# Kernel optimization log

Measured on AMD Instinct MI355X. Metric: run time of the kernel, lower is better.

## Reference

```python
import jax, jax.numpy as jnp
import numpy as np

WS = (7, 7, 7)
SS = (3, 3, 3)
SEQ = WS[0] * WS[1] * WS[2]  # 343
EPS = 1e-5


def layer_norm(x, w, b):
    mu = jnp.mean(x, axis=-1, keepdims=True)
    var = jnp.mean((x - mu) ** 2, axis=-1, keepdims=True)
    return (x - mu) * jax.lax.rsqrt(var + EPS) * w + b


def window_partition(x, ws):
    b, d, h, w, c = x.shape
    x = x.reshape(b, d // ws[0], ws[0], h // ws[1], ws[1], w // ws[2], ws[2], c)
    return x.transpose(0, 1, 3, 5, 2, 4, 6, 7).reshape(-1, ws[0] * ws[1] * ws[2], c)


def window_reverse(win, ws, dims):
    b, dp, hp, wp = dims
    x = win.reshape(b, dp // ws[0], hp // ws[1], wp // ws[2], ws[0], ws[1], ws[2], -1)
    return x.transpose(0, 1, 4, 2, 5, 3, 6, 7).reshape(b, dp, hp, wp, -1)


def _rel_pos_index():
    coords = np.stack(np.meshgrid(np.arange(WS[0]), np.arange(WS[1]), np.arange(WS[2]), indexing='ij'))
    cf = coords.reshape(3, -1)
    rel = (cf[:, :, None] - cf[:, None, :]).transpose(1, 2, 0)  # (s, s, 3)
    rel[..., 0] += WS[0] - 1
    rel[..., 1] += WS[1] - 1
    rel[..., 2] += WS[2] - 1
    idx = rel[..., 0] * (2 * WS[1] - 1) * (2 * WS[2] - 1) + rel[..., 1] * (2 * WS[2] - 1) + rel[..., 2]
    return idx.astype(np.int32)


def _swin_mask(dp, hp, wp):
    img = np.zeros((1, dp, hp, wp, 1), np.float32)
    cnt = 0
    sl = lambda ws, ss: (slice(0, -ws), slice(-ws, -ss), slice(-ss, None))
    for ds in sl(WS[0], SS[0]):
        for hs in sl(WS[1], SS[1]):
            for wsl in sl(WS[2], SS[2]):
                img[:, ds, hs, wsl, :] = cnt
                cnt += 1
    mw = np.asarray(window_partition(jnp.asarray(img), WS)).squeeze(-1)  # (nW, s)
    am = mw[:, None, :] - mw[:, :, None]
    return np.where(am != 0, np.float32(-100.0), np.float32(0.0))


def setup_inputs() -> dict:
    key = jax.random.key(0)
    ks = jax.random.split(key, 12)
    B, D, H, W, C = 1, 28, 56, 28, 192
    NH, DH = 6, 32
    FFI = 4 * C
    L = 2
    s = 0.02
    inp = {
        'x': jax.random.normal(ks[0], (B, D, H, W, C), jnp.float32),
        'mask_matrix': jnp.asarray(_swin_mask(D, H, W)),
        'clinical': jax.random.normal(ks[1], (B, 8), jnp.float32),
        'ln1_w': jnp.ones((L, C)), 'ln1_b': jnp.zeros((L, C)),
        'qkv_w': jax.random.normal(ks[2], (L, C, 3 * C)) * s, 'qkv_b': jnp.zeros((L, 3 * C)),
        'out_w': jax.random.normal(ks[3], (L, C, C)) * s, 'out_b': jnp.zeros((L, C)),
        'ln2_w': jnp.ones((L, C)), 'ln2_b': jnp.zeros((L, C)),
        'ff1_w': jax.random.normal(ks[4], (L, C, 2 * FFI)) * s, 'ff1_b': jnp.zeros((L, 2 * FFI)),
        'ff2_w': jax.random.normal(ks[5], (L, FFI, C)) * s, 'ff2_b': jnp.zeros((L, C)),
        'rpb': jax.random.normal(ks[6], (L, (2 * WS[0] - 1) * (2 * WS[1] - 1) * (2 * WS[2] - 1), NH)) * s,
        'lnf_w': jnp.ones((C,)), 'lnf_b': jnp.zeros((C,)),
        'rel_index': jnp.asarray(_rel_pos_index()),
    }
    return inp


def reference(x, mask_matrix, clinical, ln1_w, ln1_b, qkv_w, qkv_b, out_w, out_b,
              ln2_w, ln2_b, ff1_w, ff1_b, ff2_w, ff2_b, rpb, lnf_w, lnf_b, rel_index):
    b, d, h, w, c = x.shape
    nh = rpb.shape[-1]
    dh = c // nh
    # pad to window multiples (no-op for chosen shapes, kept for fidelity)
    pd = (WS[0] - d % WS[0]) % WS[0]
    ph = (WS[1] - h % WS[1]) % WS[1]
    pw = (WS[2] - w % WS[2]) % WS[2]
    xp = jnp.pad(x, ((0, 0), (0, pd), (0, ph), (0, pw), (0, 0)))
    dp, hp, wp = d + pd, h + ph, w + pw
    # cyclic shift
    xs = jnp.roll(xp, shift=(-SS[0], -SS[1], -SS[2]), axis=(1, 2, 3))
    xw = window_partition(xs, WS)  # (nW*b, s, c)
    # mask: values {0,-100} -> allowed bool (True = attend), per source math
    allowed = jnp.logical_not((mask_matrix * (-1.0 / 100.0)).astype(bool))[:, None, :, :]
    scale = 1.0 / jnp.sqrt(jnp.asarray(dh, xw.dtype))
    for l in range(2):
        hdn = layer_norm(xw, ln1_w[l], ln1_b[l])
        qkv = hdn @ qkv_w[l] + qkv_b[l]
        q, k, v = jnp.split(qkv, 3, axis=-1)
        q = q.reshape(-1, SEQ, nh, dh).transpose(0, 2, 1, 3)
        k = k.reshape(-1, SEQ, nh, dh).transpose(0, 2, 1, 3)
        v = v.reshape(-1, SEQ, nh, dh).transpose(0, 2, 1, 3)
        scores = jnp.einsum('whqd,whkd->whqk', q, k) * scale
        bias = rpb[l][rel_index].transpose(2, 0, 1)  # (nh, s, s)
        scores = scores + bias[None]
        scores = jnp.where(allowed, scores, jnp.asarray(-1e9, scores.dtype))
        attn = jax.nn.softmax(scores, axis=-1)
        o = jnp.einsum('whqk,whkd->whqd', attn, v).transpose(0, 2, 1, 3).reshape(-1, SEQ, c)
        xw = xw + (o @ out_w[l] + out_b[l])
        f = layer_norm(xw, ln2_w[l], ln2_b[l]) @ ff1_w[l] + ff1_b[l]
        u, g = jnp.split(f, 2, axis=-1)  # GLU feed-forward
        xw = xw + ((u * jax.nn.gelu(g)) @ ff2_w[l] + ff2_b[l])
    xw = layer_norm(xw, lnf_w, lnf_b)
    aw = xw.reshape(-1, WS[0], WS[1], WS[2], c)
    xs = window_reverse(aw, WS, (b, dp, hp, wp))
    xo = jnp.roll(xs, shift=(SS[0], SS[1], SS[2]), axis=(1, 2, 3))
    return xo[:, :d, :h, :w, :]
```

## Files before the change

### kernel.cpp

```cpp
#include <hip/hip_runtime.h>
#include <hip/hip_fp16.h>
#include <math.h>

#define SEQ 343
#define CCH 192
#define NWIN 128
#define NHEAD 6
#define TOK (NWIN * SEQ)

typedef __bf16 bf16x8 __attribute__((ext_vector_type(8)));
typedef float f32x4 __attribute__((ext_vector_type(4)));
typedef float f32x16 __attribute__((ext_vector_type(16)));
typedef unsigned short ushort8 __attribute__((ext_vector_type(8)));
typedef _Float16 half8 __attribute__((ext_vector_type(8)));
typedef _Float16 half4 __attribute__((ext_vector_type(4)));

__device__ __forceinline__ unsigned short f2bf(float f) {
    unsigned u = __float_as_uint(f);
    u += 0x7FFF + ((u >> 16) & 1);
    return (unsigned short)(u >> 16);
}

__device__ __forceinline__ float gelu_tanh(float x) {
    const float k0 = 0.7978845608028654f;
    const float k1 = 0.044715f;
    float y = k0 * (x + k1 * x * x * x);
    float t = 1.0f - 2.0f / (__expf(2.0f * y) + 1.0f);
    return 0.5f * x * (1.0f + t);
}

__device__ __forceinline__ void gld16(void* l, const void* g) {
    __builtin_amdgcn_global_load_lds((const __attribute__((address_space(1))) unsigned int*)g,
                                     (__attribute__((address_space(3))) unsigned int*)l, 16, 0, 0);
}

__global__ __launch_bounds__(256) void k_shift_part(const float* __restrict__ x,
                                                    float* __restrict__ xw) {
    int idx = blockIdx.x * 256 + threadIdx.x;
    if (idx >= TOK * 48) return;
    int c4 = idx % 48;
    int tok = idx / 48;
    int t = tok % SEQ;
    int wn = tok / SEQ;
    int tw = t % 7, th = (t / 7) % 7, td = t / 49;
    int ww = wn & 3, wh = (wn >> 2) & 7, wd = wn >> 5;
    int sd = (wd * 7 + td + 3) % 28;
    int sh = (wh * 7 + th + 3) % 56;
    int sw = (ww * 7 + tw + 3) % 28;
    const float4* src = (const float4*)(x + (size_t)((sd * 56 + sh) * 28 + sw) * CCH);
    ((float4*)xw)[idx] = src[c4];
}

__global__ __launch_bounds__(256) void k_ln_bf(const float* __restrict__ in,
                                               const float* __restrict__ w,
                                               const float* __restrict__ b,
                                               unsigned short* __restrict__ out, int rows) {
    int row = blockIdx.x * 4 + (threadIdx.x >> 6);
    int lane = threadIdx.x & 63;
    if (row >= rows) return;
    const float* p = in + (size_t)row * CCH;
    float v0 = p[lane], v1 = p[lane + 64], v2 = p[lane + 128];
    float s = v0 + v1 + v2;
#pragma unroll
    for (int off = 32; off > 0; off >>= 1) s += __shfl_xor(s, off);
    float mu = s * (1.0f / 192.0f);
    float d0 = v0 - mu, d1 = v1 - mu, d2 = v2 - mu;
    float vv = d0 * d0 + d1 * d1 + d2 * d2;
#pragma unroll
    for (int off = 32; off > 0; off >>= 1) vv += __shfl_xor(vv, off);
    float rs = rsqrtf(vv * (1.0f / 192.0f) + 1e-5f);
    unsigned short* q = out + (size_t)row * CCH;
    q[lane] = f2bf(d0 * rs * w[lane] + b[lane]);
    q[lane + 64] = f2bf(d1 * rs * w[lane + 64] + b[lane + 64]);
    q[lane + 128] = f2bf(d2 * rs * w[lane + 128] + b[lane + 128]);
}

__global__ __launch_bounds__(256) void k_ln_out(const float* __restrict__ xw,
                                                const float* __restrict__ w,
                                                const float* __restrict__ b,
                                                float* __restrict__ out) {
    int row = blockIdx.x * 4 + (threadIdx.x >> 6);
    int lane = threadIdx.x & 63;
    if (row >= TOK) return;
    int d = row / 1568;
    int hh = (row / 28) % 56;
    int wv = row % 28;
    int sd = (d + 25) % 28, sh = (hh + 53) % 56, sw = (wv + 25) % 28;
    int wn = (sd / 7) * 32 + (sh / 7) * 4 + (sw / 7);
    int t = (sd % 7) * 49 + (sh % 7) * 7 + (sw % 7);
    const float* p = xw + ((size_t)wn * SEQ + t) * CCH;
    float v0 = p[lane], v1 = p[lane + 64], v2 = p[lane + 128];
    float s = v0 + v1 + v2;
#pragma unroll
    for (int off = 32; off > 0; off >>= 1) s += __shfl_xor(s, off);
    float mu = s * (1.0f / 192.0f);
    float d0 = v0 - mu, d1 = v1 - mu, d2 = v2 - mu;
    float vv = d0 * d0 + d1 * d1 + d2 * d2;
#pragma unroll
    for (int off = 32; off > 0; off >>= 1) vv += __shfl_xor(vv, off);
    float rs = rsqrtf(vv * (1.0f / 192.0f) + 1e-5f);
    float* q = out + (size_t)row * CCH;
    q[lane] = d0 * rs * w[lane] + b[lane];
    q[lane + 64] = d1 * rs * w[lane + 64] + b[lane + 64];
    q[lane + 128] = d2 * rs * w[lane + 128] + b[lane + 128];
}

__global__ __launch_bounds__(256) void k_wprep(const float* __restrict__ qkv_w,
                                               const float* __restrict__ out_w,
                                               const float* __restrict__ ff1_w,
                                               const float* __restrict__ ff2_w,
                                               unsigned short* __restrict__ wt) {
    int idx = blockIdx.x * 256 + threadIdx.x;
    if (idx >= 1179648) return;
    int l = idx / 589824;
    int r = idx - l * 589824;
    const float* src;
    int Kd, Nd, off;
    if (r < 110592)      { src = qkv_w + (size_t)l * 110592; Kd = 192; Nd = 576;  off = r; }
    else if (r < 147456) { src = out_w + (size_t)l * 36864;  Kd = 192; Nd = 192;  off = r - 110592; }
    else if (r < 442368) { src = ff1_w + (size_t)l * 294912; Kd = 192; Nd = 1536; off = r - 147456; }
    else                 { src = ff2_w + (size_t)l * 147456; Kd = 768; Nd = 192;  off = r - 442368; }
    int n = off / Kd, k = off - n * Kd;
    wt[idx] = f2bf(src[(size_t)k * Nd + n]);
}

__global__ void k_cbgen2(const float* __restrict__ mask, const float* __restrict__ rpb,
                         unsigned* __restrict__ cb) {
    int q = threadIdx.x;
    int kp = blockIdx.x;
    int h = blockIdx.y;
    int cl = blockIdx.z;
    int wn = ((cl & 4) ? 96 : 0) + ((cl & 2) ? 28 : 0) + ((cl & 1) ? 3 : 0);
    const float LOG2E = 1.4426950408889634f;
    int qd = q / 49, qh = (q / 7) % 7, qw = q % 7;
    unsigned short v[2];
#pragma unroll
    for (int t = 0; t < 2; ++t) {
        int k = 2 * kp + t;
        float val = -14000.0f;
        if (k < SEQ && q < SEQ) {
            float mk = mask[((size_t)wn * SEQ + k) * SEQ + q];
            if (mk == 0.0f) {
                int kd = k / 49, kh = (k / 7) % 7, kw = k % 7;
                int rel = (qd - kd + 6) * 169 + (qh - kh + 6) * 13 + (qw - kw + 6);
                val = rpb[(size_t)rel * NHEAD + h] * LOG2E;
            }
        }
        v[t] = __half_as_ushort(__float2half_rn(val));
    }
    cb[((size_t)(cl * NHEAD + h) * 176 + kp) * 352 + q] = (unsigned)v[0] | ((unsigned)v[1] << 16);
}

template <int MODE>
__global__ __launch_bounds__(256) void k_gemm32(const unsigned short* __restrict__ A,
                                                const unsigned short* __restrict__ Wt,
                                                const float* __restrict__ bias,
                                                float* __restrict__ outF,
                                                unsigned short* __restrict__ outB,
                                                _Float16* __restrict__ outH,
                                                _Float16* __restrict__ outV,
                                                int N, int K) {
    constexpr int BN = (MODE == 0) ? 192 : 64;
    constexpr int NF = (MODE == 0) ? 3 : 1;
    constexpr int WNC = NF * 32;
    constexpr int BROWS = (MODE == 0) ? 192 : ((MODE == 2) ? 128 : 64);
    constexpr int BCH = (BROWS * 128) / 4096;
    __shared__ char AsB[16384];
    __shared__ char BsB[BROWS * 128];
    const int tid = threadIdx.x;
    const int n0 = blockIdx.x * BN;
    const size_t m0 = (size_t)blockIdx.y * 128;
    const int lane = tid & 63, wid = tid >> 6;
    const int wm = wid >> 1, wn = wid & 1;
    const int ln31 = lane & 31, hi16 = (lane >> 5) * 16;
    const int xorv = (ln31 & 7) << 4;
    const size_t ldb = (size_t)K * 2;

    f32x16 acc[2][NF];
    f32x16 accG[2];
#pragma unroll
    for (int mi = 0; mi < 2; ++mi) {
#pragma unroll
        for (int nj = 0; nj < NF; ++nj) acc[mi][nj] = (f32x16)(0.f);
        accG[mi] = (f32x16)(0.f);
    }

    for (int kb = 0; kb < K; kb += 64) {
#pragma unroll
        for (int i = 0; i < 4; ++i) {
            int s = i * 4096 + tid * 16;
            int r = s >> 7;
            int cb = (s & 127) ^ ((r & 7) << 4);
            gld16(AsB + s, (const char*)A + (m0 + r) * ldb + (size_t)kb * 2 + cb);
        }
#pragma unroll
        for (int i = 0; i < BCH; ++i) {
            int s = i * 4096 + tid * 16;
            int r = s >> 7;
            int cb = (s & 127) ^ ((r & 7) << 4);
            int grow = n0 + r + ((MODE == 2 && r >= 64) ? 704 : 0);
            gld16(BsB + s, (const char*)Wt + (size_t)grow * ldb + (size_t)kb * 2 + cb);
        }
        __syncthreads();
#pragma unroll
        for (int ks = 0; ks < 4; ++ks) {
            const int ccb = (ks * 32 + hi16) ^ xorv;
            bf16x8 a0 = *(const bf16x8*)(AsB + (wm * 64 + ln31) * 128 + ccb);
            bf16x8 a1 = *(const bf16x8*)(AsB + (wm * 64 + 32 + ln31) * 128 + ccb);
            if (MODE == 2) {
                bf16x8 bu = *(const bf16x8*)(BsB + (wn * 32 + ln31) * 128 + ccb);
                bf16x8 bg = *(const bf16x8*)(BsB + (64 + wn * 32 + ln31) * 128 + ccb);
                acc[0][0] = __builtin_amdgcn_mfma_f32_32x32x16_bf16(a0, bu, acc[0][0], 0, 0, 0);
                acc[1][0] = __builtin_amdgcn_mfma_f32_32x32x16_bf16(a1, bu, acc[1][0], 0, 0, 0);
                accG[0] = __builtin_amdgcn_mfma_f32_32x32x16_bf16(a0, bg, accG[0], 0, 0, 0);
                accG[1] = __builtin_amdgcn_mfma_f32_32x32x16_bf16(a1, bg, accG[1], 0, 0, 0);
            } else {
#pragma unroll
                for (int nj = 0; nj < NF; ++nj) {
                    bf16x8 b = *(const bf16x8*)(BsB + (wn * WNC + nj * 32 + ln31) * 128 + ccb);
                    acc[0][nj] = __builtin_amdgcn_mfma_f32_32x32x16_bf16(a0, b, acc[0][nj], 0, 0, 0);
                    acc[1][nj] = __builtin_amdgcn_mfma_f32_32x32x16_bf16(a1, b, acc[1][nj], 0, 0, 0);
                }
            }
        }
        __syncthreads();
    }

    const float S2LOG = 0.17677669529663687f * 1.4426950408889634f;
    const int rbase = (int)m0 + wm * 64 + ((lane >> 5) << 2);
    const int cbase = n0 + wn * WNC + ln31;
#pragma unroll
    for (int mi = 0; mi < 2; ++mi) {
#pragma unroll
        for (int nj = 0; nj < NF; ++nj) {
            const int gc = cbase + nj * 32;
            const float bb = bias[gc];
            const float bgv = (MODE == 2) ? bias[768 + gc] : 0.f;
#pragma unroll
            for (int reg = 0; reg < 16; ++reg) {
                const int row = rbase + mi * 32 + (reg & 3) + ((reg >> 2) << 3);
                float v = acc[mi][nj][reg] + bb;
                if (MODE == 1) {
                    outF[(size_t)row * N + gc] += v;
                } else if (MODE == 0) {
                    if (n0 < 384) {
                        outH[(size_t)row * 384 + gc] = (_Float16)(n0 == 0 ? v * S2LOG : v);
                    } else {
                        int d = gc - 384, hh = d >> 5, dd = d & 31;
                        int wnn = row / 343, qq = row - wnn * 343;
                        outV[(((size_t)wnn * NHEAD + hh) * 32 + dd) * 344 + qq] = (_Float16)v;
                    }
                } else {
                    float g = accG[mi][reg] + bgv;
                    outB[(size_t)row * 768 + gc] = f2bf(v * gelu_tanh(g));
                }
            }
        }
    }
}

__global__ __launch_bounds__(256) void k_attn3(const _Float16* __restrict__ qk,
                                               const _Float16* __restrict__ vt,
                                               const unsigned* __restrict__ cb,
                                               unsigned short* __restrict__ o) {
    __shared__ _Float16 Ks[352][40];
    __shared__ _Float16 Vt[32][360];
    __shared__ _Float16 Pb[4][48][16][4];
    const int h = blockIdx.x;
    const int wn = blockIdx.y;
    const int tid = threadIdx.x;
    const _Float16* kbase = qk + (size_t)wn * SEQ * 384 + 192 + h * 32;
    for (int j = tid; j < 352 * 4; j += 256) {
        int s = j >> 2, c = (j & 3) * 8;
        half8 v = {};
        if (s < SEQ) v = *(const half8*)&kbase[(size_t)s * 384 + c];
        *(half8*)&Ks[s][c] = v;
    }
    const _Float16* vbase = vt + ((size_t)wn * NHEAD + h) * 32 * 344;
    for (int j = tid; j < 32 * 44; j += 256) {
        int d = j / 44, c = (j % 44) * 8;
        half8 v = {};
        if (c + 7 <= 342) {
            v = *(const half8*)&vbase[(size_t)d * 344 + c];
        } else if (c <= 342) {
#pragma unroll
            for (int i = 0; i < 8; ++i) v[i] = (c + i <= 342) ? vbase[(size_t)d * 344 + c + i] : (_Float16)0.f;
        }
        *(half8*)&Vt[d][c] = v;
    }
    __syncthreads();
    const int wid = tid >> 6, lane = tid & 63;
    const int qloc = lane & 15, g = lane >> 4;
    int cls = (((wn >> 5) == 3) ? 4 : 0) | ((((wn >> 2) & 7) == 7) ? 2 : 0) | (((wn & 3) == 3) ? 1 : 0);
    const unsigned* cbb = cb + (size_t)(cls * NHEAD + h) * 176 * 352;
    for (int qt = wid; qt < 22; qt += 4) {
        const int q0 = qt * 16;
        const int qrow = q0 + qloc;
        half8 qf = {};
        if (qrow < SEQ) qf = *(const half8*)&qk[((size_t)wn * SEQ + qrow) * 384 + h * 32 + g * 8];
        f32x4 st[22];
#pragma unroll
        for (int kt = 0; kt < 22; ++kt) {
            half8 kf = *(const half8*)&Ks[kt * 16 + qloc][g * 8];
            st[kt] = __builtin_amdgcn_mfma_f32_16x16x32_f16(kf, qf, (f32x4){0.f, 0.f, 0.f, 0.f}, 0, 0, 0);
        }
        float m = -1e30f;
#pragma unroll
        for (int kt = 0; kt < 22; ++kt) {
            const unsigned* cp = cbb + (size_t)(kt * 8 + g * 2) * 352 + q0 + qloc;
            unsigned b0 = cp[0];
            unsigned b1 = cp[352];
            __half2 h0 = *(__half2*)&b0, h1 = *(__half2*)&b1;
            st[kt][0] += __low2float(h0);
            st[kt][1] += __high2float(h0);
            st[kt][2] += __low2float(h1);
            st[kt][3] += __high2float(h1);
            m = fmaxf(m, fmaxf(fmaxf(st[kt][0], st[kt][1]), fmaxf(st[kt][2], st[kt][3])));
        }
        m = fmaxf(m, __shfl_xor(m, 16));
        m = fmaxf(m, __shfl_xor(m, 32));
        float l = 0.f;
        f32x4 acc0 = {0.f, 0.f, 0.f, 0.f}, acc1 = {0.f, 0.f, 0.f, 0.f};
        asm volatile("s_waitcnt lgkmcnt(0)" ::: "memory");
#pragma unroll
        for (int kt = 0; kt < 12; ++kt) {
            float p0 = exp2f(st[kt][0] - m), p1 = exp2f(st[kt][1] - m);
            float p2 = exp2f(st[kt][2] - m), p3 = exp2f(st[kt][3] - m);
            l += (p0 + p1) + (p2 + p3);
            half4 pv = {(_Float16)p0, (_Float16)p1, (_Float16)p2, (_Float16)p3};
            *(half4*)&Pb[wid][kt * 4 + g][qloc][0] = pv;
        }
        asm volatile("s_waitcnt lgkmcnt(0)" ::: "memory");
#pragma unroll
        for (int ks = 0; ks < 6; ++ks) {
            half4 pa = *(half4*)&Pb[wid][ks * 8 + g * 2][qloc][0];
            half4 pb = *(half4*)&Pb[wid][ks * 8 + g * 2 + 1][qloc][0];
            half8 pf = {pa[0], pa[1], pa[2], pa[3], pb[0], pb[1], pb[2], pb[3]};
            half8 v0 = *(const half8*)&Vt[qloc][ks * 32 + g * 8];
            half8 v1 = *(const half8*)&Vt[16 + qloc][ks * 32 + g * 8];
            acc0 = __builtin_amdgcn_mfma_f32_16x16x32_f16(v0, pf, acc0, 0, 0, 0);
            acc1 = __builtin_amdgcn_mfma_f32_16x16x32_f16(v1, pf, acc1, 0, 0, 0);
        }
        asm volatile("s_waitcnt lgkmcnt(0)" ::: "memory");
#pragma unroll
        for (int kt = 12; kt < 22; ++kt) {
            float p0 = exp2f(st[kt][0] - m), p1 = exp2f(st[kt][1] - m);
            float p2 = exp2f(st[kt][2] - m), p3 = exp2f(st[kt][3] - m);
            l += (p0 + p1) + (p2 + p3);
            half4 pv = {(_Float16)p0, (_Float16)p1, (_Float16)p2, (_Float16)p3};
            *(half4*)&Pb[wid][(kt - 12) * 4 + g][qloc][0] = pv;
        }
        asm volatile("s_waitcnt lgkmcnt(0)" ::: "memory");
#pragma unroll
        for (int ks = 0; ks < 5; ++ks) {
            half4 pa = *(half4*)&Pb[wid][ks * 8 + g * 2][qloc][0];
            half4 pb = *(half4*)&Pb[wid][ks * 8 + g * 2 + 1][qloc][0];
            half8 pf = {pa[0], pa[1], pa[2], pa[3], pb[0], pb[1], pb[2], pb[3]};
            half8 v0 = *(const half8*)&Vt[qloc][192 + ks * 32 + g * 8];
            half8 v1 = *(const half8*)&Vt[16 + qloc][192 + ks * 32 + g * 8];
            acc0 = __builtin_amdgcn_mfma_f32_16x16x32_f16(v0, pf, acc0, 0, 0, 0);
            acc1 = __builtin_amdgcn_mfma_f32_16x16x32_f16(v1, pf, acc1, 0, 0, 0);
        }
        l += __shfl_xor(l, 16);
        l += __shfl_xor(l, 32);
        if (qrow < SEQ) {
            float inv = 1.0f / l;
            unsigned short* orow = o + ((size_t)wn * SEQ + qrow) * CCH + h * 32;
            ushort2 w0 = {f2bf(acc0[0] * inv), f2bf(acc0[1] * inv)};
            ushort2 w1 = {f2bf(acc0[2] * inv), f2bf(acc0[3] * inv)};
            ushort2 w2 = {f2bf(acc1[0] * inv), f2bf(acc1[1] * inv)};
            ushort2 w3 = {f2bf(acc1[2] * inv), f2bf(acc1[3] * inv)};
            *(ushort2*)&orow[g * 4] = w0;
            *(ushort2*)&orow[g * 4 + 2] = w1;
            *(ushort2*)&orow[16 + g * 4] = w2;
            *(ushort2*)&orow[16 + g * 4 + 2] = w3;
        }
    }
}

extern "C" void kernel_launch(void* const* d_in, const int* in_sizes, int n_in,
                              void* d_out, int out_size, void* d_ws, size_t ws_size,
                              hipStream_t stream) {
    const float* x     = (const float*)d_in[0];
    const float* mask  = (const float*)d_in[1];
    const float* ln1_w = (const float*)d_in[3];
    const float* ln1_b = (const float*)d_in[4];
    const float* qkv_w = (const float*)d_in[5];
    const float* qkv_b = (const float*)d_in[6];
    const float* out_w = (const float*)d_in[7];
    const float* out_b = (const float*)d_in[8];
    const float* ln2_w = (const float*)d_in[9];
    const float* ln2_b = (const float*)d_in[10];
    const float* ff1_w = (const float*)d_in[11];
    const float* ff1_b = (const float*)d_in[12];
    const float* ff2_w = (const float*)d_in[13];
    const float* ff2_b = (const float*)d_in[14];
    const float* rpb   = (const float*)d_in[15];
    const float* lnf_w = (const float*)d_in[16];
    const float* lnf_b = (const float*)d_in[17];

    char* wsp = (char*)d_ws;
    float* xw = (float*)wsp;                          wsp += (size_t)TOK * 192 * 4;
    unsigned short* hdnb = (unsigned short*)wsp;      wsp += (size_t)TOK * 192 * 2;
    _Float16* qkh = (_Float16*)wsp;                   wsp += (size_t)TOK * 384 * 2;
    _Float16* vth = (_Float16*)wsp;                   wsp += (size_t)NWIN * NHEAD * 32 * 344 * 2;
    unsigned short* glub = (unsigned short*)wsp;      wsp += (size_t)TOK * 768 * 2;
    unsigned short* wt = (unsigned short*)wsp;        wsp += (size_t)1179648 * 2;
    unsigned* cb = (unsigned*)wsp;
    float* out = (float*)d_out;

    k_shift_part<<<8232, 256, 0, stream>>>(x, xw);
    k_wprep<<<4608, 256, 0, stream>>>(qkv_w, out_w, ff1_w, ff2_w, wt);
    for (int l = 0; l < 2; ++l) {
        unsigned short* wbase = wt + (size_t)l * 589824;
        k_cbgen2<<<dim3(176, NHEAD, 8), 352, 0, stream>>>(mask, rpb + (size_t)l * 2197 * NHEAD, cb);
        k_ln_bf<<<10976, 256, 0, stream>>>(xw, ln1_w + l * 192, ln1_b + l * 192, hdnb, TOK);
        k_gemm32<0><<<dim3(3, 343), 256, 0, stream>>>(hdnb, wbase, qkv_b + l * 576,
                                                      nullptr, nullptr, qkh, vth, 576, 192);
        k_attn3<<<dim3(NHEAD, NWIN), 256, 0, stream>>>(qkh, vth, cb, hdnb);
        k_gemm32<1><<<dim3(3, 343), 256, 0, stream>>>(hdnb, wbase + 110592, out_b + l * 192,
                                                      xw, nullptr, nullptr, nullptr, 192, 192);
        k_ln_bf<<<10976, 256, 0, stream>>>(xw, ln2_w + l * 192, ln2_b + l * 192, hdnb, TOK);
        k_gemm32<2><<<dim3(12, 343), 256, 0, stream>>>(hdnb, wbase + 147456, ff1_b + l * 1536,
                                                       nullptr, glub, nullptr, nullptr, 768, 192);
        k_gemm32<1><<<dim3(3, 343), 256, 0, stream>>>(glub, wbase + 442368, ff2_b + l * 192,
                                                      xw, nullptr, nullptr, nullptr, 192, 768);
    }
    k_ln_out<<<10976, 256, 0, stream>>>(xw, lnf_w, lnf_b, out);
}
```

Before: 575.1 us.

## Rework window attention: packed fp16 scores, bpermute P transpose, swizzled LDS

```diff
diff --git a/kernel.cpp b/kernel.cpp
--- a/kernel.cpp
+++ b/kernel.cpp
@@ -13,7 +13,7 @@
 typedef float f32x16 __attribute__((ext_vector_type(16)));
 typedef unsigned short ushort8 __attribute__((ext_vector_type(8)));
 typedef _Float16 half8 __attribute__((ext_vector_type(8)));
-typedef _Float16 half4 __attribute__((ext_vector_type(4)));
+typedef _Float16 hv2 __attribute__((ext_vector_type(2)));
 
 __device__ __forceinline__ unsigned short f2bf(float f) {
     unsigned u = __float_as_uint(f);
@@ -33,6 +33,12 @@
     __builtin_amdgcn_global_load_lds((const __attribute__((address_space(1))) unsigned int*)g,
                                      (__attribute__((address_space(3))) unsigned int*)l, 16, 0, 0);
 }
+
+__device__ __forceinline__ hv2 pkrtz(float a, float b) {
+    return __builtin_bit_cast(hv2, __builtin_amdgcn_cvt_pkrtz(a, b));
+}
+__device__ __forceinline__ hv2 u2h2(unsigned u) { return __builtin_bit_cast(hv2, u); }
+__device__ __forceinline__ unsigned h22u(hv2 h) { return __builtin_bit_cast(unsigned, h); }
 
 __global__ __launch_bounds__(256) void k_shift_part(const float* __restrict__ x,
                                                     float* __restrict__ xw) {
@@ -124,19 +130,19 @@
     wt[idx] = f2bf(src[(size_t)k * Nd + n]);
 }
 
-__global__ void k_cbgen2(const float* __restrict__ mask, const float* __restrict__ rpb,
-                         unsigned* __restrict__ cb) {
+__global__ void k_cbgen3(const float* __restrict__ mask, const float* __restrict__ rpb,
+                         uint2* __restrict__ cb4) {
     int q = threadIdx.x;
-    int kp = blockIdx.x;
+    int k4 = blockIdx.x;
     int h = blockIdx.y;
     int cl = blockIdx.z;
     int wn = ((cl & 4) ? 96 : 0) + ((cl & 2) ? 28 : 0) + ((cl & 1) ? 3 : 0);
     const float LOG2E = 1.4426950408889634f;
     int qd = q / 49, qh = (q / 7) % 7, qw = q % 7;
-    unsigned short v[2];
-#pragma unroll
-    for (int t = 0; t < 2; ++t) {
-        int k = 2 * kp + t;
+    unsigned v[4];
+#pragma unroll
+    for (int t = 0; t < 4; ++t) {
+        int k = 4 * k4 + t;
         float val = -14000.0f;
         if (k < SEQ && q < SEQ) {
             float mk = mask[((size_t)wn * SEQ + k) * SEQ + q];
@@ -148,7 +154,8 @@
         }
         v[t] = __half_as_ushort(__float2half_rn(val));
     }
-    cb[((size_t)(cl * NHEAD + h) * 176 + kp) * 352 + q] = (unsigned)v[0] | ((unsigned)v[1] << 16);
+    uint2 pk = {v[0] | (v[1] << 16), v[2] | (v[3] << 16)};
+    cb4[((size_t)(cl * NHEAD + h) * 88 + k4) * 352 + q] = pk;
 }
 
 template <int MODE>
@@ -259,121 +266,102 @@
     }
 }
 
-__global__ __launch_bounds__(256) void k_attn3(const _Float16* __restrict__ qk,
+__global__ __launch_bounds__(256) void k_attn4(const _Float16* __restrict__ qk,
                                                const _Float16* __restrict__ vt,
-                                               const unsigned* __restrict__ cb,
+                                               const uint2* __restrict__ cb4,
                                                unsigned short* __restrict__ o) {
-    __shared__ _Float16 Ks[352][40];
-    __shared__ _Float16 Vt[32][360];
-    __shared__ _Float16 Pb[4][48][16][4];
+    __shared__ _Float16 Ks[352 * 32];
+    __shared__ _Float16 Vt[32 * 352];
     const int h = blockIdx.x;
     const int wn = blockIdx.y;
     const int tid = threadIdx.x;
     const _Float16* kbase = qk + (size_t)wn * SEQ * 384 + 192 + h * 32;
-    for (int j = tid; j < 352 * 4; j += 256) {
-        int s = j >> 2, c = (j & 3) * 8;
-        half8 v = {};
-        if (s < SEQ) v = *(const half8*)&kbase[(size_t)s * 384 + c];
-        *(half8*)&Ks[s][c] = v;
+    for (int j = tid; j < 1408; j += 256) {
+        int s = j >> 2, c = j & 3;
+        int slot = c ^ ((s >> 2) & 3);
+        *(half8*)&Ks[s * 32 + slot * 8] = *(const half8*)&kbase[(size_t)s * 384 + c * 8];
     }
     const _Float16* vbase = vt + ((size_t)wn * NHEAD + h) * 32 * 344;
-    for (int j = tid; j < 32 * 44; j += 256) {
-        int d = j / 44, c = (j % 44) * 8;
-        half8 v = {};
-        if (c + 7 <= 342) {
-            v = *(const half8*)&vbase[(size_t)d * 344 + c];
-        } else if (c <= 342) {
-#pragma unroll
-            for (int i = 0; i < 8; ++i) v[i] = (c + i <= 342) ? vbase[(size_t)d * 344 + c + i] : (_Float16)0.f;
-        }
-        *(half8*)&Vt[d][c] = v;
+    for (int j = tid; j < 1408; j += 256) {
+        int d = j / 44, ch = j % 44;
+        int slot = ch ^ ((d >> 2) & 3);
+        *(half8*)&Vt[d * 352 + slot * 8] = *(const half8*)&vbase[(size_t)d * 344 + ch * 8];
     }
     __syncthreads();
     const int wid = tid >> 6, lane = tid & 63;
     const int qloc = lane & 15, g = lane >> 4;
+    const int xq = (qloc >> 2) & 3;
+    const int slotK = (g ^ xq) * 8;
+    const int iA = (qloc | ((g & 1) << 5)) * 4;
+    const int iB = iA + 64;
+    const bool ghi = g >= 2;
     int cls = (((wn >> 5) == 3) ? 4 : 0) | ((((wn >> 2) & 7) == 7) ? 2 : 0) | (((wn & 3) == 3) ? 1 : 0);
-    const unsigned* cbb = cb + (size_t)(cls * NHEAD + h) * 176 * 352;
+    const uint2* cbb = cb4 + (size_t)(cls * NHEAD + h) * 88 * 352;
     for (int qt = wid; qt < 22; qt += 4) {
         const int q0 = qt * 16;
         const int qrow = q0 + qloc;
-        half8 qf = {};
-        if (qrow < SEQ) qf = *(const half8*)&qk[((size_t)wn * SEQ + qrow) * 384 + h * 32 + g * 8];
-        f32x4 st[22];
+        half8 qf = *(const half8*)&qk[((size_t)wn * SEQ + qrow) * 384 + h * 32 + g * 8];
+        unsigned spk[22][2];
+        hv2 mpk = {(_Float16)(-60000.0f), (_Float16)(-60000.0f)};
+        __builtin_amdgcn_s_setprio(1);
 #pragma unroll
         for (int kt = 0; kt < 22; ++kt) {
-            half8 kf = *(const half8*)&Ks[kt * 16 + qloc][g * 8];
-            st[kt] = __builtin_amdgcn_mfma_f32_16x16x32_f16(kf, qf, (f32x4){0.f, 0.f, 0.f, 0.f}, 0, 0, 0);
-        }
-        float m = -1e30f;
+            half8 kf = *(const half8*)&Ks[(kt * 16 + qloc) * 32 + slotK];
+            f32x4 st = __builtin_amdgcn_mfma_f32_16x16x32_f16(kf, qf, (f32x4){0.f, 0.f, 0.f, 0.f}, 0, 0, 0);
+            uint2 cv = cbb[(size_t)(kt * 4 + g) * 352 + qrow];
+            hv2 s01 = pkrtz(st[0], st[1]) + u2h2(cv.x);
+            hv2 s23 = pkrtz(st[2], st[3]) + u2h2(cv.y);
+            mpk = __builtin_elementwise_max(mpk, __builtin_elementwise_max(s01, s23));
+            spk[kt][0] = h22u(s01);
+            spk[kt][1] = h22u(s23);
+        }
+        __builtin_amdgcn_s_setprio(0);
+        float mf = fmaxf((float)mpk[0], (float)mpk[1]);
+        mf = fmaxf(mf, __shfl_xor(mf, 16));
+        mf = fmaxf(mf, __shfl_xor(mf, 32));
+        float l = 0.f;
 #pragma unroll
         for (int kt = 0; kt < 22; ++kt) {
-            const unsigned* cp = cbb + (size_t)(kt * 8 + g * 2) * 352 + q0 + qloc;
-            unsigned b0 = cp[0];
-            unsigned b1 = cp[352];
-            __half2 h0 = *(__half2*)&b0, h1 = *(__half2*)&b1;
-            st[kt][0] += __low2float(h0);
-            st[kt][1] += __high2float(h0);
-            st[kt][2] += __low2float(h1);
-            st[kt][3] += __high2float(h1);
-            m = fmaxf(m, fmaxf(fmaxf(st[kt][0], st[kt][1]), fmaxf(st[kt][2], st[kt][3])));
-        }
-        m = fmaxf(m, __shfl_xor(m, 16));
-        m = fmaxf(m, __shfl_xor(m, 32));
-        float l = 0.f;
+            hv2 s01 = u2h2(spk[kt][0]);
+            hv2 s23 = u2h2(spk[kt][1]);
+            float e0 = exp2f((float)s01[0] - mf), e1 = exp2f((float)s01[1] - mf);
+            float e2 = exp2f((float)s23[0] - mf), e3 = exp2f((float)s23[1] - mf);
+            l += (e0 + e1) + (e2 + e3);
+            spk[kt][0] = h22u(pkrtz(e0, e1));
+            spk[kt][1] = h22u(pkrtz(e2, e3));
+        }
+        l += __shfl_xor(l, 16);
+        l += __shfl_xor(l, 32);
         f32x4 acc0 = {0.f, 0.f, 0.f, 0.f}, acc1 = {0.f, 0.f, 0.f, 0.f};
-        asm volatile("s_waitcnt lgkmcnt(0)" ::: "memory");
-#pragma unroll
-        for (int kt = 0; kt < 12; ++kt) {
-            float p0 = exp2f(st[kt][0] - m), p1 = exp2f(st[kt][1] - m);
-            float p2 = exp2f(st[kt][2] - m), p3 = exp2f(st[kt][3] - m);
-            l += (p0 + p1) + (p2 + p3);
-            half4 pv = {(_Float16)p0, (_Float16)p1, (_Float16)p2, (_Float16)p3};
-            *(half4*)&Pb[wid][kt * 4 + g][qloc][0] = pv;
-        }
-        asm volatile("s_waitcnt lgkmcnt(0)" ::: "memory");
-#pragma unroll
-        for (int ks = 0; ks < 6; ++ks) {
-            half4 pa = *(half4*)&Pb[wid][ks * 8 + g * 2][qloc][0];
-            half4 pb = *(half4*)&Pb[wid][ks * 8 + g * 2 + 1][qloc][0];
-            half8 pf = {pa[0], pa[1], pa[2], pa[3], pb[0], pb[1], pb[2], pb[3]};
-            half8 v0 = *(const half8*)&Vt[qloc][ks * 32 + g * 8];
-            half8 v1 = *(const half8*)&Vt[16 + qloc][ks * 32 + g * 8];
+        __builtin_amdgcn_s_setprio(1);
+#pragma unroll
+        for (int ch = 0; ch < 11; ++ch) {
+            unsigned a0 = __builtin_amdgcn_ds_bpermute(iA, spk[2 * ch][0]);
+            unsigned a1 = __builtin_amdgcn_ds_bpermute(iA, spk[2 * ch][1]);
+            unsigned a2 = __builtin_amdgcn_ds_bpermute(iB, spk[2 * ch][0]);
+            unsigned a3 = __builtin_amdgcn_ds_bpermute(iB, spk[2 * ch][1]);
+            unsigned b0 = __builtin_amdgcn_ds_bpermute(iA, spk[2 * ch + 1][0]);
+            unsigned b1 = __builtin_amdgcn_ds_bpermute(iA, spk[2 * ch + 1][1]);
+            unsigned b2 = __builtin_amdgcn_ds_bpermute(iB, spk[2 * ch + 1][0]);
+            unsigned b3 = __builtin_amdgcn_ds_bpermute(iB, spk[2 * ch + 1][1]);
+            uint4 pfu = {ghi ? b0 : a0, ghi ? b1 : a1, ghi ? b2 : a2, ghi ? b3 : a3};
+            half8 pf = __builtin_bit_cast(half8, pfu);
+            const int slotV = ((ch * 4 + g) ^ xq) * 8;
+            half8 v0 = *(const half8*)&Vt[qloc * 352 + slotV];
+            half8 v1 = *(const half8*)&Vt[(qloc + 16) * 352 + slotV];
             acc0 = __builtin_amdgcn_mfma_f32_16x16x32_f16(v0, pf, acc0, 0, 0, 0);
             acc1 = __builtin_amdgcn_mfma_f32_16x16x32_f16(v1, pf, acc1, 0, 0, 0);
         }
-        asm volatile("s_waitcnt lgkmcnt(0)" ::: "memory");
-#pragma unroll
-        for (int kt = 12; kt < 22; ++kt) {
-            float p0 = exp2f(st[kt][0] - m), p1 = exp2f(st[kt][1] - m);
-            float p2 = exp2f(st[kt][2] - m), p3 = exp2f(st[kt][3] - m);
-            l += (p0 + p1) + (p2 + p3);
-            half4 pv = {(_Float16)p0, (_Float16)p1, (_Float16)p2, (_Float16)p3};
-            *(half4*)&Pb[wid][(kt - 12) * 4 + g][qloc][0] = pv;
-        }
-        asm volatile("s_waitcnt lgkmcnt(0)" ::: "memory");
-#pragma unroll
-        for (int ks = 0; ks < 5; ++ks) {
-            half4 pa = *(half4*)&Pb[wid][ks * 8 + g * 2][qloc][0];
-            half4 pb = *(half4*)&Pb[wid][ks * 8 + g * 2 + 1][qloc][0];
-            half8 pf = {pa[0], pa[1], pa[2], pa[3], pb[0], pb[1], pb[2], pb[3]};
-            half8 v0 = *(const half8*)&Vt[qloc][192 + ks * 32 + g * 8];
-            half8 v1 = *(const half8*)&Vt[16 + qloc][192 + ks * 32 + g * 8];
-            acc0 = __builtin_amdgcn_mfma_f32_16x16x32_f16(v0, pf, acc0, 0, 0, 0);
-            acc1 = __builtin_amdgcn_mfma_f32_16x16x32_f16(v1, pf, acc1, 0, 0, 0);
-        }
-        l += __shfl_xor(l, 16);
-        l += __shfl_xor(l, 32);
+        __builtin_amdgcn_s_setprio(0);
         if (qrow < SEQ) {
             float inv = 1.0f / l;
             unsigned short* orow = o + ((size_t)wn * SEQ + qrow) * CCH + h * 32;
-            ushort2 w0 = {f2bf(acc0[0] * inv), f2bf(acc0[1] * inv)};
-            ushort2 w1 = {f2bf(acc0[2] * inv), f2bf(acc0[3] * inv)};
-            ushort2 w2 = {f2bf(acc1[0] * inv), f2bf(acc1[1] * inv)};
-            ushort2 w3 = {f2bf(acc1[2] * inv), f2bf(acc1[3] * inv)};
-            *(ushort2*)&orow[g * 4] = w0;
-            *(ushort2*)&orow[g * 4 + 2] = w1;
-            *(ushort2*)&orow[16 + g * 4] = w2;
-            *(ushort2*)&orow[16 + g * 4 + 2] = w3;
+            ushort4 w0 = {f2bf(acc0[0] * inv), f2bf(acc0[1] * inv),
+                          f2bf(acc0[2] * inv), f2bf(acc0[3] * inv)};
+            ushort4 w1 = {f2bf(acc1[0] * inv), f2bf(acc1[1] * inv),
+                          f2bf(acc1[2] * inv), f2bf(acc1[3] * inv)};
+            *(ushort4*)&orow[g * 4] = w0;
+            *(ushort4*)&orow[16 + g * 4] = w1;
         }
     }
 }
@@ -406,18 +394,18 @@
     _Float16* vth = (_Float16*)wsp;                   wsp += (size_t)NWIN * NHEAD * 32 * 344 * 2;
     unsigned short* glub = (unsigned short*)wsp;      wsp += (size_t)TOK * 768 * 2;
     unsigned short* wt = (unsigned short*)wsp;        wsp += (size_t)1179648 * 2;
-    unsigned* cb = (unsigned*)wsp;
+    uint2* cb4 = (uint2*)wsp;
     float* out = (float*)d_out;
 
     k_shift_part<<<8232, 256, 0, stream>>>(x, xw);
     k_wprep<<<4608, 256, 0, stream>>>(qkv_w, out_w, ff1_w, ff2_w, wt);
     for (int l = 0; l < 2; ++l) {
         unsigned short* wbase = wt + (size_t)l * 589824;
-        k_cbgen2<<<dim3(176, NHEAD, 8), 352, 0, stream>>>(mask, rpb + (size_t)l * 2197 * NHEAD, cb);
+        k_cbgen3<<<dim3(88, NHEAD, 8), 352, 0, stream>>>(mask, rpb + (size_t)l * 2197 * NHEAD, cb4);
         k_ln_bf<<<10976, 256, 0, stream>>>(xw, ln1_w + l * 192, ln1_b + l * 192, hdnb, TOK);
         k_gemm32<0><<<dim3(3, 343), 256, 0, stream>>>(hdnb, wbase, qkv_b + l * 576,
                                                       nullptr, nullptr, qkh, vth, 576, 192);
-        k_attn3<<<dim3(NHEAD, NWIN), 256, 0, stream>>>(qkh, vth, cb, hdnb);
+        k_attn4<<<dim3(NHEAD, NWIN), 256, 0, stream>>>(qkh, vth, cb4, hdnb);
         k_gemm32<1><<<dim3(3, 343), 256, 0, stream>>>(hdnb, wbase + 110592, out_b + l * 192,
                                                       xw, nullptr, nullptr, nullptr, 192, 192);
         k_ln_bf<<<10976, 256, 0, stream>>>(xw, ln2_w + l * 192, ln2_b + l * 192, hdnb, TOK);
```

Measured after the change: 694.6 us. 20.8% more time.

## Prefetch next K-tile into registers while computing current tile in GEMM

Applied to the files above, without the earlier changes.

```diff
diff --git a/kernel.cpp b/kernel.cpp
--- a/kernel.cpp
+++ b/kernel.cpp
@@ -185,23 +185,44 @@
         accG[mi] = (f32x16)(0.f);
     }
 
+#pragma unroll
+    for (int i = 0; i < 4; ++i) {
+        int s = i * 4096 + tid * 16;
+        int r = s >> 7;
+        int cbx = (s & 127) ^ ((r & 7) << 4);
+        gld16(AsB + s, (const char*)A + (m0 + r) * ldb + cbx);
+    }
+#pragma unroll
+    for (int i = 0; i < BCH; ++i) {
+        int s = i * 4096 + tid * 16;
+        int r = s >> 7;
+        int cbx = (s & 127) ^ ((r & 7) << 4);
+        int grow = n0 + r + ((MODE == 2 && r >= 64) ? 704 : 0);
+        gld16(BsB + s, (const char*)Wt + (size_t)grow * ldb + cbx);
+    }
+    __syncthreads();
+
     for (int kb = 0; kb < K; kb += 64) {
-#pragma unroll
-        for (int i = 0; i < 4; ++i) {
-            int s = i * 4096 + tid * 16;
-            int r = s >> 7;
-            int cb = (s & 127) ^ ((r & 7) << 4);
-            gld16(AsB + s, (const char*)A + (m0 + r) * ldb + (size_t)kb * 2 + cb);
-        }
-#pragma unroll
-        for (int i = 0; i < BCH; ++i) {
-            int s = i * 4096 + tid * 16;
-            int r = s >> 7;
-            int cb = (s & 127) ^ ((r & 7) << 4);
-            int grow = n0 + r + ((MODE == 2 && r >= 64) ? 704 : 0);
-            gld16(BsB + s, (const char*)Wt + (size_t)grow * ldb + (size_t)kb * 2 + cb);
-        }
-        __syncthreads();
+        const bool more = (kb + 64) < K;
+        uint4 ra[4], rb[BCH];
+        if (more) {
+            const size_t ko = (size_t)(kb + 64) * 2;
+#pragma unroll
+            for (int i = 0; i < 4; ++i) {
+                int s = i * 4096 + tid * 16;
+                int r = s >> 7;
+                int cbx = (s & 127) ^ ((r & 7) << 4);
+                ra[i] = *(const uint4*)((const char*)A + (m0 + r) * ldb + ko + cbx);
+            }
+#pragma unroll
+            for (int i = 0; i < BCH; ++i) {
+                int s = i * 4096 + tid * 16;
+                int r = s >> 7;
+                int cbx = (s & 127) ^ ((r & 7) << 4);
+                int grow = n0 + r + ((MODE == 2 && r >= 64) ? 704 : 0);
+                rb[i] = *(const uint4*)((const char*)Wt + (size_t)grow * ldb + ko + cbx);
+            }
+        }
 #pragma unroll
         for (int ks = 0; ks < 4; ++ks) {
             const int ccb = (ks * 32 + hi16) ^ xorv;
@@ -223,7 +244,14 @@
                 }
             }
         }
-        __syncthreads();
+        if (more) {
+            __syncthreads();
+#pragma unroll
+            for (int i = 0; i < 4; ++i) *(uint4*)(AsB + i * 4096 + tid * 16) = ra[i];
+#pragma unroll
+            for (int i = 0; i < BCH; ++i) *(uint4*)(BsB + i * 4096 + tid * 16) = rb[i];
+            __syncthreads();
+        }
     }
 
     const float S2LOG = 0.17677669529663687f * 1.4426950408889634f;
```

Result: slower. 929.5 us (+61.6%).

## Store Q and K in MFMA fragment-ready tiled layout, drop K shared-memory staging

Applied to the files above, without the earlier changes.

```diff
diff --git a/kernel.cpp b/kernel.cpp
--- a/kernel.cpp
+++ b/kernel.cpp
@@ -124,6 +124,17 @@
     wt[idx] = f2bf(src[(size_t)k * Nd + n]);
 }
 
+__global__ void k_zfill(_Float16* __restrict__ qT, _Float16* __restrict__ kT) {
+    int wh = blockIdx.x;
+    int t = threadIdx.x;
+    int qloc = 7 + t / 32;
+    int c = t % 32;
+    int g = c >> 3, c8 = c & 7;
+    size_t off = (size_t)wh * 11264 + 21 * 512 + g * 128 + qloc * 8 + c8;
+    qT[off] = (_Float16)0.f;
+    kT[off] = (_Float16)0.f;
+}
+
 __global__ void k_cbgen2(const float* __restrict__ mask, const float* __restrict__ rpb,
                          unsigned* __restrict__ cb) {
     int q = threadIdx.x;
@@ -157,7 +168,8 @@
                                                 const float* __restrict__ bias,
                                                 float* __restrict__ outF,
                                                 unsigned short* __restrict__ outB,
-                                                _Float16* __restrict__ outH,
+                                                _Float16* __restrict__ qT,
+                                                _Float16* __restrict__ kT,
                                                 _Float16* __restrict__ outV,
                                                 int N, int K) {
     constexpr int BN = (MODE == 0) ? 192 : 64;
@@ -190,16 +202,16 @@
         for (int i = 0; i < 4; ++i) {
             int s = i * 4096 + tid * 16;
             int r = s >> 7;
-            int cb = (s & 127) ^ ((r & 7) << 4);
-            gld16(AsB + s, (const char*)A + (m0 + r) * ldb + (size_t)kb * 2 + cb);
+            int cbx = (s & 127) ^ ((r & 7) << 4);
+            gld16(AsB + s, (const char*)A + (m0 + r) * ldb + (size_t)kb * 2 + cbx);
         }
 #pragma unroll
         for (int i = 0; i < BCH; ++i) {
             int s = i * 4096 + tid * 16;
             int r = s >> 7;
-            int cb = (s & 127) ^ ((r & 7) << 4);
+            int cbx = (s & 127) ^ ((r & 7) << 4);
             int grow = n0 + r + ((MODE == 2 && r >= 64) ? 704 : 0);
-            gld16(BsB + s, (const char*)Wt + (size_t)grow * ldb + (size_t)kb * 2 + cb);
+            gld16(BsB + s, (const char*)Wt + (size_t)grow * ldb + (size_t)kb * 2 + cbx);
         }
         __syncthreads();
 #pragma unroll
@@ -243,11 +255,19 @@
                 if (MODE == 1) {
                     outF[(size_t)row * N + gc] += v;
                 } else if (MODE == 0) {
-                    if (n0 < 384) {
-                        outH[(size_t)row * 384 + gc] = (_Float16)(n0 == 0 ? v * S2LOG : v);
+                    int wnn = row / 343, qq = row - wnn * 343;
+                    if (gc < 192) {
+                        int hh = gc >> 5, c = gc & 31;
+                        int qt = qq >> 4, ql = qq & 15, gg = c >> 3, c8 = c & 7;
+                        qT[(size_t)(wnn * NHEAD + hh) * 11264 + qt * 512 + gg * 128 + ql * 8 + c8] =
+                            (_Float16)(v * S2LOG);
+                    } else if (gc < 384) {
+                        int d = gc - 192, hh = d >> 5, c = d & 31;
+                        int kt2 = qq >> 4, ql = qq & 15, gg = c >> 3, c8 = c & 7;
+                        kT[(size_t)(wnn * NHEAD + hh) * 11264 + kt2 * 512 + gg * 128 + ql * 8 + c8] =
+                            (_Float16)v;
                     } else {
                         int d = gc - 384, hh = d >> 5, dd = d & 31;
-                        int wnn = row / 343, qq = row - wnn * 343;
                         outV[(((size_t)wnn * NHEAD + hh) * 32 + dd) * 344 + qq] = (_Float16)v;
                     }
                 } else {
@@ -259,23 +279,16 @@
     }
 }
 
-__global__ __launch_bounds__(256) void k_attn3(const _Float16* __restrict__ qk,
+__global__ __launch_bounds__(256) void k_attn6(const _Float16* __restrict__ qT,
+                                               const _Float16* __restrict__ kT,
                                                const _Float16* __restrict__ vt,
                                                const unsigned* __restrict__ cb,
                                                unsigned short* __restrict__ o) {
-    __shared__ _Float16 Ks[352][40];
     __shared__ _Float16 Vt[32][360];
     __shared__ _Float16 Pb[4][48][16][4];
     const int h = blockIdx.x;
     const int wn = blockIdx.y;
     const int tid = threadIdx.x;
-    const _Float16* kbase = qk + (size_t)wn * SEQ * 384 + 192 + h * 32;
-    for (int j = tid; j < 352 * 4; j += 256) {
-        int s = j >> 2, c = (j & 3) * 8;
-        half8 v = {};
-        if (s < SEQ) v = *(const half8*)&kbase[(size_t)s * 384 + c];
-        *(half8*)&Ks[s][c] = v;
-    }
     const _Float16* vbase = vt + ((size_t)wn * NHEAD + h) * 32 * 344;
     for (int j = tid; j < 32 * 44; j += 256) {
         int d = j / 44, c = (j % 44) * 8;
@@ -291,17 +304,18 @@
     __syncthreads();
     const int wid = tid >> 6, lane = tid & 63;
     const int qloc = lane & 15, g = lane >> 4;
+    const _Float16* qb = qT + (size_t)(wn * NHEAD + h) * 11264;
+    const _Float16* kb = kT + (size_t)(wn * NHEAD + h) * 11264;
     int cls = (((wn >> 5) == 3) ? 4 : 0) | ((((wn >> 2) & 7) == 7) ? 2 : 0) | (((wn & 3) == 3) ? 1 : 0);
     const unsigned* cbb = cb + (size_t)(cls * NHEAD + h) * 176 * 352;
     for (int qt = wid; qt < 22; qt += 4) {
         const int q0 = qt * 16;
         const int qrow = q0 + qloc;
-        half8 qf = {};
-        if (qrow < SEQ) qf = *(const half8*)&qk[((size_t)wn * SEQ + qrow) * 384 + h * 32 + g * 8];
+        half8 qf = *(const half8*)&qb[qt * 512 + lane * 8];
         f32x4 st[22];
 #pragma unroll
         for (int kt = 0; kt < 22; ++kt) {
-            half8 kf = *(const half8*)&Ks[kt * 16 + qloc][g * 8];
+            half8 kf = *(const half8*)&kb[kt * 512 + lane * 8];
             st[kt] = __builtin_amdgcn_mfma_f32_16x16x32_f16(kf, qf, (f32x4){0.f, 0.f, 0.f, 0.f}, 0, 0, 0);
         }
         float m = -1e30f;
@@ -402,7 +416,8 @@
     char* wsp = (char*)d_ws;
     float* xw = (float*)wsp;                          wsp += (size_t)TOK * 192 * 4;
     unsigned short* hdnb = (unsigned short*)wsp;      wsp += (size_t)TOK * 192 * 2;
-    _Float16* qkh = (_Float16*)wsp;                   wsp += (size_t)TOK * 384 * 2;
+    _Float16* qTh = (_Float16*)wsp;                   wsp += (size_t)768 * 11264 * 2;
+    _Float16* kTh = (_Float16*)wsp;                   wsp += (size_t)768 * 11264 * 2;
     _Float16* vth = (_Float16*)wsp;                   wsp += (size_t)NWIN * NHEAD * 32 * 344 * 2;
     unsigned short* glub = (unsigned short*)wsp;      wsp += (size_t)TOK * 768 * 2;
     unsigned short* wt = (unsigned short*)wsp;        wsp += (size_t)1179648 * 2;
@@ -411,20 +426,21 @@
 
     k_shift_part<<<8232, 256, 0, stream>>>(x, xw);
     k_wprep<<<4608, 256, 0, stream>>>(qkv_w, out_w, ff1_w, ff2_w, wt);
+    k_zfill<<<768, 288, 0, stream>>>(qTh, kTh);
     for (int l = 0; l < 2; ++l) {
         unsigned short* wbase = wt + (size_t)l * 589824;
         k_cbgen2<<<dim3(176, NHEAD, 8), 352, 0, stream>>>(mask, rpb + (size_t)l * 2197 * NHEAD, cb);
         k_ln_bf<<<10976, 256, 0, stream>>>(xw, ln1_w + l * 192, ln1_b + l * 192, hdnb, TOK);
         k_gemm32<0><<<dim3(3, 343), 256, 0, stream>>>(hdnb, wbase, qkv_b + l * 576,
-                                                      nullptr, nullptr, qkh, vth, 576, 192);
-        k_attn3<<<dim3(NHEAD, NWIN), 256, 0, stream>>>(qkh, vth, cb, hdnb);
+                                                      nullptr, nullptr, qTh, kTh, vth, 576, 192);
+        k_attn6<<<dim3(NHEAD, NWIN), 256, 0, stream>>>(qTh, kTh, vth, cb, hdnb);
         k_gemm32<1><<<dim3(3, 343), 256, 0, stream>>>(hdnb, wbase + 110592, out_b + l * 192,
-                                                      xw, nullptr, nullptr, nullptr, 192, 192);
+                                                      xw, nullptr, nullptr, nullptr, nullptr, 192, 192);
         k_ln_bf<<<10976, 256, 0, stream>>>(xw, ln2_w + l * 192, ln2_b + l * 192, hdnb, TOK);
         k_gemm32<2><<<dim3(12, 343), 256, 0, stream>>>(hdnb, wbase + 147456, ff1_b + l * 1536,
-                                                       nullptr, glub, nullptr, nullptr, 768, 192);
+                                                       nullptr, glub, nullptr, nullptr, nullptr, 768, 192);
         k_gemm32<1><<<dim3(3, 343), 256, 0, stream>>>(glub, wbase + 442368, ff2_b + l * 192,
-                                                      xw, nullptr, nullptr, nullptr, 192, 768);
+                                                      xw, nullptr, nullptr, nullptr, nullptr, 192, 768);
     }
     k_ln_out<<<10976, 256, 0, stream>>>(xw, lnf_w, lnf_b, out);
 }
```

New measurement: 675.0 us. 1.17x slower.
